# Kernel tuning notes

Measured on AMD Instinct MI355X. Metric: run time of the kernel, lower is better.

## Reference

```python
import jax, jax.numpy as jnp
from jax import lax
import numpy as np

B, H, W = 2, 48, 48
C_IN, C_OUT = 96, 192
D_INNER, N_STATE, DT_RANK, K = 192, 16, 6, 4  # VMamba: expand=2, d_state=16, dt_rank=ceil(C/16)
EPS = 1e-5


def setup_inputs() -> dict:
    ks = jax.random.split(jax.random.key(0), 16)
    s = 0.02
    r = lambda k, sh, sc=s: jax.random.normal(k, sh, jnp.float32) * sc
    d, N, R = D_INNER, N_STATE, DT_RANK
    return {
        "x": jax.random.normal(ks[0], (B, C_IN, H, W), jnp.float32),
        "ln_g": jnp.ones((C_IN,), jnp.float32),
        "ln_b": jnp.zeros((C_IN,), jnp.float32),
        "in_proj_w": r(ks[1], (2 * d, C_IN)),
        "dwconv_w": r(ks[2], (d, 1, 3, 3)),
        "dwconv_b": jnp.zeros((d,), jnp.float32),
        "x_proj_w": r(ks[3], (K, R + 2 * N, d)),
        "dt_w": r(ks[4], (K, d, R)),
        "dt_b": r(ks[5], (K, d), 0.1),
        "A_logs": jnp.tile(jnp.log(jnp.arange(1, N + 1, dtype=jnp.float32)), (K, d, 1)),
        "Ds": jnp.ones((K, d), jnp.float32),
        "out_norm_g": jnp.ones((d,), jnp.float32),
        "out_norm_b": jnp.zeros((d,), jnp.float32),
        "out_proj_w": r(ks[6], (C_IN, d)),
        "w1": r(ks[7], (C_OUT, C_IN, 1, 1)),
        "b1": jnp.zeros((C_OUT,), jnp.float32),
        "w31": r(ks[8], (C_OUT, C_IN, 3, 3)),
        "b31": jnp.zeros((C_OUT,), jnp.float32),
        "w32": r(ks[9], (C_OUT, C_IN, 3, 3)),
        "b32": jnp.zeros((C_OUT,), jnp.float32),
        "w33": r(ks[10], (C_OUT, C_OUT, 3, 3)),
        "b33": jnp.zeros((C_OUT,), jnp.float32),
        "bn_g": jnp.ones((3 * C_OUT,), jnp.float32),
        "bn_b": jnp.zeros((3 * C_OUT,), jnp.float32),
        "bn_m": r(ks[11], (3 * C_OUT,), 0.1),
        "bn_v": jax.random.uniform(ks[12], (3 * C_OUT,), jnp.float32) + 0.5,
        "prelu_a": jnp.float32(0.25),
    }


def _layernorm(x, g, b):
    m = jnp.mean(x, -1, keepdims=True)
    v = jnp.var(x, -1, keepdims=True)
    return (x - m) * lax.rsqrt(v + EPS) * g + b


def _conv(x, w, b, stride, pad, groups=1):
    y = lax.conv_general_dilated(x, w, (stride, stride), [(pad, pad), (pad, pad)],
                                 dimension_numbers=("NCHW", "OIHW", "NCHW"),
                                 feature_group_count=groups)
    return y + b[None, :, None, None]


def _ss2d(x, in_proj_w, dwconv_w, dwconv_b, x_proj_w, dt_w, dt_b, A_logs, Ds,
          out_norm_g, out_norm_b, out_proj_w):
    # x: (B, H, W, C)
    Bb, Hh, Ww, C = x.shape
    d, N, R = D_INNER, N_STATE, DT_RANK
    L = Hh * Ww
    xz = jnp.einsum("bhwc,ec->bhwe", x, in_proj_w)  # (B,H,W,2d)
    xin, z = jnp.split(xz, 2, axis=-1)
    xc = jnp.transpose(xin, (0, 3, 1, 2))           # (B,d,H,W)
    xc = jax.nn.silu(_conv(xc, dwconv_w, dwconv_b, 1, 1, groups=d))
    # 4 scan directions: row-major, col-major, and their reverses
    x_flat = xc.reshape(Bb, d, L)
    x_t = jnp.transpose(xc, (0, 1, 3, 2)).reshape(Bb, d, L)
    xs = jnp.stack([x_flat, x_t, x_flat[:, :, ::-1], x_t[:, :, ::-1]], axis=1)  # (B,K,d,L)
    x_dbl = jnp.einsum("bkdl,kcd->bkcl", xs, x_proj_w)
    dts, Bs, Cs = x_dbl[:, :, :R], x_dbl[:, :, R:R + N], x_dbl[:, :, R + N:]
    delta = jax.nn.softplus(jnp.einsum("bkrl,kdr->bkdl", dts, dt_w) + dt_b[None, :, :, None])
    A = -jnp.exp(A_logs)                                   # (K,d,N)
    dA = jnp.exp(jnp.einsum("bkdl,kdn->lbkdn", delta, A))  # (L,B,K,d,N)
    dBu = jnp.einsum("bkdl,bknl,bkdl->lbkdn", delta, Bs, xs)
    Cseq = jnp.transpose(Cs, (3, 0, 1, 2))                 # (L,B,K,N)

    def step(h, inp):
        dA_t, dBu_t, c_t = inp
        h = dA_t * h + dBu_t
        return h, jnp.einsum("bkdn,bkn->bkd", h, c_t)

    h0 = jnp.zeros((Bb, K, d, N), x.dtype)
    _, ys = lax.scan(step, h0, (dA, dBu, Cseq))            # ys: (L,B,K,d)
    ys = jnp.transpose(ys, (1, 2, 3, 0)) + xs * Ds[None, :, :, None]  # (B,K,d,L)

    def t_back(a):  # undo the HW transpose of col-major scans
        return jnp.transpose(a.reshape(Bb, d, Ww, Hh), (0, 1, 3, 2)).reshape(Bb, d, L)

    y = ys[:, 0] + ys[:, 2, :, ::-1] + t_back(ys[:, 1]) + t_back(ys[:, 3, :, ::-1])
    y = _layernorm(jnp.transpose(y, (0, 2, 1)), out_norm_g, out_norm_b).reshape(Bb, Hh, Ww, d)
    y = y * jax.nn.silu(z)
    return jnp.einsum("bhwd,cd->bhwc", y, out_proj_w)


def reference(x, ln_g, ln_b, in_proj_w, dwconv_w, dwconv_b, x_proj_w, dt_w, dt_b,
              A_logs, Ds, out_norm_g, out_norm_b, out_proj_w,
              w1, b1, w31, b31, w32, b32, w33, b33,
              bn_g, bn_b, bn_m, bn_v, prelu_a):
    # VSSBlock: residual + SS2D on LayerNorm'd NHWC features
    x_nhwc = jnp.transpose(x, (0, 2, 3, 1))
    x_nhwc = x_nhwc + _ss2d(_layernorm(x_nhwc, ln_g, ln_b), in_proj_w, dwconv_w,
                            dwconv_b, x_proj_w, dt_w, dt_b, A_logs, Ds,
                            out_norm_g, out_norm_b, out_proj_w)
    xm = jnp.transpose(x_nhwc, (0, 3, 1, 2))  # (B,C,H,W)
    # multi-branch stride-2 downsample
    x1 = _conv(xm, w1, b1, 2, 0)
    x2 = _conv(xm, w31, b31, 2, 1)
    x3 = _conv(_conv(xm, w32, b32, 2, 1), w33, b33, 1, 1)
    out = jnp.concatenate([x1, x2, x3], axis=1)  # (B, 3*C_OUT, H/2, W/2)
    # BatchNorm2d (inference, running stats) + PReLU(single param)
    out = (out - bn_m[None, :, None, None]) * lax.rsqrt(bn_v + EPS)[None, :, None, None] \
          * bn_g[None, :, None, None] + bn_b[None, :, None, None]
    return jnp.where(out > 0, out, prelu_a * out)
```

## Files before the change

### kernel.cpp

```cpp
#include <hip/hip_runtime.h>
#include <math.h>

#define BB_ 2
#define HH 48
#define WW 48
#define LL 2304
#define CIN 96
#define DD 192
#define KK 4
#define NN 16
#define RR 6
#define NCH 96
#define LC 24
#define COUT 192
#define OH 24
#define OW 24
#define OHW 576
#define NPX 1152
#define NTOT 4608
#define EPSF 1e-5f

typedef __attribute__((ext_vector_type(8))) short bf16x8;
typedef __attribute__((ext_vector_type(4))) float f32x4;

__device__ __forceinline__ short f2bf(float f) {
  unsigned u = __float_as_uint(f);
  unsigned r = (u + 0x7fffu + ((u >> 16) & 1u)) >> 16;
  return (short)r;
}

__global__ __launch_bounds__(256) void k_prep(const float* __restrict__ x,
                                              const float* __restrict__ g,
                                              const float* __restrict__ b,
                                              const float* __restrict__ inw,
                                              const float* __restrict__ xpw,
                                              const float* __restrict__ w31,
                                              const float* __restrict__ w32,
                                              const float* __restrict__ w33,
                                              const float* __restrict__ w1,
                                              const float* __restrict__ wout,
                                              float* __restrict__ stats,
                                              float* __restrict__ WgT,
                                              float* __restrict__ sWg,
                                              float* __restrict__ sWb,
                                              short* __restrict__ At3b,
                                              short* __restrict__ At1b,
                                              short* __restrict__ At2b,
                                              short* __restrict__ woutb) {
  int bx = blockIdx.x;
  int tid = threadIdx.x;
  if (bx < 72) {
    int bb = bx / 36; int l0 = (bx % 36) * 64;
    int p = tid >> 2, q = tid & 3;
    int l = l0 + p;
    const float* xp = x + bb * CIN * LL + l;
    float s = 0.f, ss = 0.f;
    for (int c = q; c < CIN; c += 4) { float v = xp[c * LL]; s += v; ss += v * v; }
    s += __shfl_xor(s, 1, 64); s += __shfl_xor(s, 2, 64);
    ss += __shfl_xor(ss, 1, 64); ss += __shfl_xor(ss, 2, 64);
    if (q == 0) {
      float m = s / CIN; float var = ss / CIN - m * m;
      stats[(bb * LL + l) * 2 + 0] = m;
      stats[(bb * LL + l) * 2 + 1] = rsqrtf(var + EPSF);
    }
  } else if (bx == 72) {
    for (int e = tid; e < 2 * DD; e += 256) {
      float swg = 0.f, swb = 0.f;
      for (int c = 0; c < CIN; c++) {
        float w = inw[e * CIN + c];
        float wg = w * g[c];
        WgT[c * 384 + e] = wg;
        swg += wg; swb += w * b[c];
      }
      sWg[e] = swg; sWb[e] = swb;
    }
  } else if (bx < 217) {
    int idx = (bx - 73) * 256 + tid;
    if (idx < 192 * 192) {
      int m = idx / 192;
      At3b[idx] = (m < 152) ? f2bf(xpw[idx]) : (short)0;
    }
  } else if (bx < 2161) {
    int i = (bx - 217) * 256 + tid;
    if (i < 497664) {
      float v;
      if (i < 165888) v = w31[i];
      else if (i < 331776) v = w32[i - 165888];
      else {
        int k = i % 864; int m = i / 864 - 384;
        v = (k % 9 == 4) ? w1[m * 96 + k / 9] : 0.f;
      }
      At1b[i] = f2bf(v);
    }
  } else if (bx < 3457) {
    int i = (bx - 2161) * 256 + tid;
    if (i < 331776) At2b[i] = f2bf(w33[i]);
  } else {
    int i = (bx - 3457) * 256 + tid;
    if (i < 18432) woutb[i] = f2bf(wout[i]);
  }
}

__global__ __launch_bounds__(256) void k_dwconv(const float* __restrict__ xin,
                                                const float* __restrict__ wdw,
                                                const float* __restrict__ bdw,
                                                float* __restrict__ xs,
                                                short* __restrict__ xsb) {
  __shared__ float vt[32 * 50];
  int bid = blockIdx.x;
  int bb = bid / 288; int r = bid % 288; int dg = r / 72; int tile = r % 72;
  int l0 = tile * 32;
  int d0 = dg * 48;
  for (int i = threadIdx.x; i < 32 * 48; i += 256) {
    int lj = i & 31, dl = i >> 5;
    int d = d0 + dl;
    int l = l0 + lj;
    int h = l / WW, w = l % WW;
    const float* xp = xin + (bb * DD + d) * LL;
    const float* wq = wdw + d * 9;
    float acc = bdw[d];
#pragma unroll
    for (int kh = 0; kh < 3; kh++) {
      int ih = h + kh - 1; if (ih < 0 || ih >= HH) continue;
#pragma unroll
      for (int kw = 0; kw < 3; kw++) {
        int iw = w + kw - 1; if (iw < 0 || iw >= WW) continue;
        acc += xp[ih * WW + iw] * wq[kh * 3 + kw];
      }
    }
    float v = acc / (1.f + __expf(-acc));
    vt[lj * 50 + dl] = v;
  }
  __syncthreads();
  for (int j = threadIdx.x; j < 32 * 48; j += 256) {
    int lj = j / 48, dl = j - lj * 48;
    int d = d0 + dl;
    int l = l0 + lj;
    int h = l / WW, w = l % WW;
    int lt = w * HH + h;
    float v = vt[lj * 50 + dl];
    xs[((size_t)(bb * 2 + 0) * LL + l) * DD + d] = v;
    xs[((size_t)(bb * 2 + 1) * LL + lt) * DD + d] = v;
    xsb[((size_t)bb * LL + l) * DD + d] = f2bf(v);
  }
}

__global__ __launch_bounds__(256) void k_xprojF(const short* __restrict__ At3b,
                                                const short* __restrict__ xsb,
                                                const float* __restrict__ dtw,
                                                const float* __restrict__ dtb,
                                                float* __restrict__ Bsb,
                                                float* __restrict__ Csb,
                                                float* __restrict__ delta) {
  __shared__ short As[192][40];
  __shared__ short Bs[32][40];
  __shared__ float ct[152][33];
  int p0 = blockIdx.x * 32;
  int tid = threadIdx.x;
  int lane = tid & 63;
  int wv = tid >> 6;
  int row16 = lane & 15;
  int kg = lane >> 4;
  f32x4 acc[3][2];
#pragma unroll
  for (int j = 0; j < 3; j++)
#pragma unroll
    for (int nf = 0; nf < 2; nf++) acc[j][nf] = (f32x4){0.f, 0.f, 0.f, 0.f};
  for (int ks = 0; ks < 192; ks += 32) {
#pragma unroll
    for (int it = 0; it < 3; it++) {
      int slot = tid + 256 * it;
      int sm = slot >> 2, sk8 = (slot & 3) * 8;
      *(bf16x8*)&As[sm][sk8] = *(const bf16x8*)&At3b[(size_t)sm * 192 + ks + sk8];
    }
    if (tid < 128) {
      int sn = tid >> 2, sk8 = (tid & 3) * 8;
      *(bf16x8*)&Bs[sn][sk8] = *(const bf16x8*)&xsb[(size_t)(p0 + sn) * 192 + ks + sk8];
    }
    __syncthreads();
#pragma unroll
    for (int j = 0; j < 3; j++) {
      bf16x8 a = *(const bf16x8*)&As[(wv * 3 + j) * 16 + row16][kg * 8];
#pragma unroll
      for (int nf = 0; nf < 2; nf++) {
        bf16x8 b = *(const bf16x8*)&Bs[nf * 16 + row16][kg * 8];
        acc[j][nf] = __builtin_amdgcn_mfma_f32_16x16x32_bf16(a, b, acc[j][nf], 0, 0, 0);
      }
    }
    __syncthreads();
  }
#pragma unroll
  for (int j = 0; j < 3; j++) {
    int rowb = (wv * 3 + j) * 16 + kg * 4;
#pragma unroll
    for (int nf = 0; nf < 2; nf++) {
      int col = nf * 16 + row16;
#pragma unroll
      for (int i = 0; i < 4; i++) {
        int r = rowb + i;
        if (r < 152) ct[r][col] = acc[j][nf][i];
      }
    }
  }
  __syncthreads();
  int bb = p0 / LL;
  int lbase = p0 - bb * LL;
  for (int i = tid; i < 2048; i += 256) {
    int k = i >> 9; int rem = i & 511; int lj = rem >> 4; int n = rem & 15;
    int l = lbase + lj; int h = l / WW, w = l - h * WW; int lt = w * HH + h;
    int pos = (k == 0) ? l : (k == 1) ? lt : (k == 2) ? (LL - 1 - l) : (LL - 1 - lt);
    size_t base = ((size_t)(bb * 4 + k) * LL + pos) * NN + n;
    Bsb[base] = ct[k * 38 + 6 + n][lj];
    Csb[base] = ct[k * 38 + 22 + n][lj];
  }
  for (int k = 0; k < 4; k++) {
    for (int i = tid; i < 32 * 192; i += 256) {
      int lj = i / 192, d = i - lj * 192;
      int l = lbase + lj; int h = l / WW, w = l - h * WW; int lt = w * HH + h;
      int pos = (k == 0) ? l : (k == 1) ? lt : (k == 2) ? (LL - 1 - l) : (LL - 1 - lt);
      const float* wd = dtw + (k * DD + d) * RR;
      float a2 = dtb[k * DD + d];
#pragma unroll
      for (int r = 0; r < RR; r++) a2 += wd[r] * ct[k * 38 + r][lj];
      float sp = a2 > 20.f ? a2 : log1pf(__expf(a2));
      delta[((size_t)(bb * 4 + k) * LL + pos) * DD + d] = sp;
    }
  }
}

__global__ __launch_bounds__(192) void k_scan1(const float* __restrict__ delta,
                                               const float* __restrict__ xs,
                                               const float* __restrict__ Bsb,
                                               const float* __restrict__ A_logs,
                                               float* __restrict__ Pbuf,
                                               float* __restrict__ Sbuf) {
  __shared__ float Bls[LC * NN];
  int bid = blockIdx.x;
  int c = bid % NCH; int bk = bid / NCH; int k = bk & 3; int bb = bk >> 2;
  int t0 = c * LC;
  int d = threadIdx.x;
  const float* bp = Bsb + ((size_t)bk * LL + t0) * NN;
  for (int i = d; i < LC * NN; i += 192) Bls[i] = bp[i];
  float A[NN];
  {
    const float4* ap = (const float4*)(A_logs + (k * DD + d) * NN);
#pragma unroll
    for (int j = 0; j < 4; j++) {
      float4 a4 = ap[j];
      A[4 * j + 0] = -__expf(a4.x); A[4 * j + 1] = -__expf(a4.y);
      A[4 * j + 2] = -__expf(a4.z); A[4 * j + 3] = -__expf(a4.w);
    }
  }
  bool seq = true;
#pragma unroll
  for (int n = 0; n < NN; n++) seq = seq && (fabsf(A[n] + (float)(n + 1)) < 1e-3f);
  float h[NN];
#pragma unroll
  for (int n = 0; n < NN; n++) h[n] = 0.f;
  float sd = 0.f;
  __syncthreads();
  const float* dp = delta + ((size_t)bk * LL + t0) * DD + d;
  const float* xpb = xs + ((size_t)(bb * 2 + (k & 1)) * LL) * DD + d;
  const float* xp; int xstep;
  if (k < 2) { xp = xpb + (size_t)t0 * DD; xstep = DD; }
  else       { xp = xpb + (size_t)(LL - 1 - t0) * DD; xstep = -DD; }
#pragma unroll 2
  for (int t = 0; t < LC; ++t) {
    float dt = dp[t * DD];
    float xv = xp[t * xstep];
    float u = dt * xv;
    sd += dt;
    float dA[NN];
    if (seq) {
      float q = __expf(-dt);
      float q2 = q * q, q4 = q2 * q2, q8 = q4 * q4;
      dA[0] = q; dA[1] = q2; dA[2] = q2 * q; dA[3] = q4;
      dA[4] = q4 * q; dA[5] = q4 * q2; dA[6] = q4 * dA[2]; dA[7] = q8;
      dA[8] = q8 * q; dA[9] = q8 * q2; dA[10] = q8 * dA[2]; dA[11] = q8 * q4;
      dA[12] = q8 * dA[4]; dA[13] = q8 * dA[5]; dA[14] = q8 * dA[6]; dA[15] = q8 * q8;
    } else {
#pragma unroll
      for (int n = 0; n < NN; n++) dA[n] = __expf(dt * A[n]);
    }
    const float4* b4 = (const float4*)&Bls[t * NN];
#pragma unroll
    for (int j = 0; j < 4; j++) {
      float4 bv = b4[j];
      h[4 * j + 0] = dA[4 * j + 0] * h[4 * j + 0] + u * bv.x;
      h[4 * j + 1] = dA[4 * j + 1] * h[4 * j + 1] + u * bv.y;
      h[4 * j + 2] = dA[4 * j + 2] * h[4 * j + 2] + u * bv.z;
      h[4 * j + 3] = dA[4 * j + 3] * h[4 * j + 3] + u * bv.w;
    }
  }
  int chn = (bk * DD + d) * NN;
  float* pp = Pbuf + (size_t)c * 24576 + chn;
  float* sp = Sbuf + (size_t)c * 24576 + chn;
#pragma unroll
  for (int n = 0; n < NN; n++) { pp[n] = __expf(A[n] * sd); sp[n] = h[n]; }
}

__global__ __launch_bounds__(256) void k_scan2(const float* __restrict__ Pbuf,
                                               const float* __restrict__ Sbuf,
                                               float* __restrict__ Hinit) {
  int idx = blockIdx.x * 256 + threadIdx.x;
  float h = 0.f;
  for (int c = 0; c < NCH; c++) {
    Hinit[(size_t)c * 24576 + idx] = h;
    h = Pbuf[(size_t)c * 24576 + idx] * h + Sbuf[(size_t)c * 24576 + idx];
  }
}

__global__ __launch_bounds__(192) void k_scan3(const float* __restrict__ delta,
                                               const float* __restrict__ xs,
                                               const float* __restrict__ Bsb,
                                               const float* __restrict__ Csb,
                                               const float* __restrict__ A_logs,
                                               const float* __restrict__ Ds,
                                               const float* __restrict__ Hinit,
                                               float* __restrict__ ys) {
  __shared__ float Bls[LC * NN];
  __shared__ float Cls[LC * NN];
  int bid = blockIdx.x;
  int c = bid % NCH; int bk = bid / NCH; int k = bk & 3; int bb = bk >> 2;
  int t0 = c * LC;
  int d = threadIdx.x;
  const float* bp = Bsb + ((size_t)bk * LL + t0) * NN;
  const float* cp = Csb + ((size_t)bk * LL + t0) * NN;
  for (int i = d; i < LC * NN; i += 192) { Bls[i] = bp[i]; Cls[i] = cp[i]; }
  float A[NN];
  {
    const float4* ap = (const float4*)(A_logs + (k * DD + d) * NN);
#pragma unroll
    for (int j = 0; j < 4; j++) {
      float4 a4 = ap[j];
      A[4 * j + 0] = -__expf(a4.x); A[4 * j + 1] = -__expf(a4.y);
      A[4 * j + 2] = -__expf(a4.z); A[4 * j + 3] = -__expf(a4.w);
    }
  }
  bool seq = true;
#pragma unroll
  for (int n = 0; n < NN; n++) seq = seq && (fabsf(A[n] + (float)(n + 1)) < 1e-3f);
  float Dv = Ds[k * DD + d];
  float h[NN];
  {
    const float4* hp = (const float4*)(Hinit + (size_t)c * 24576 + (bk * DD + d) * NN);
#pragma unroll
    for (int j = 0; j < 4; j++) {
      float4 h4 = hp[j];
      h[4 * j + 0] = h4.x; h[4 * j + 1] = h4.y;
      h[4 * j + 2] = h4.z; h[4 * j + 3] = h4.w;
    }
  }
  __syncthreads();
  const float* dp = delta + ((size_t)bk * LL + t0) * DD + d;
  const float* xpb = xs + ((size_t)(bb * 2 + (k & 1)) * LL) * DD + d;
  const float* xp; int xstep;
  if (k < 2) { xp = xpb + (size_t)t0 * DD; xstep = DD; }
  else       { xp = xpb + (size_t)(LL - 1 - t0) * DD; xstep = -DD; }
  float* yp = ys + ((size_t)bk * LL + t0) * DD + d;
#pragma unroll 2
  for (int t = 0; t < LC; ++t) {
    float dt = dp[t * DD];
    float xv = xp[t * xstep];
    float u = dt * xv;
    float y = 0.f;
    float dA[NN];
    if (seq) {
      float q = __expf(-dt);
      float q2 = q * q, q4 = q2 * q2, q8 = q4 * q4;
      dA[0] = q; dA[1] = q2; dA[2] = q2 * q; dA[3] = q4;
      dA[4] = q4 * q; dA[5] = q4 * q2; dA[6] = q4 * dA[2]; dA[7] = q8;
      dA[8] = q8 * q; dA[9] = q8 * q2; dA[10] = q8 * dA[2]; dA[11] = q8 * q4;
      dA[12] = q8 * dA[4]; dA[13] = q8 * dA[5]; dA[14] = q8 * dA[6]; dA[15] = q8 * q8;
    } else {
#pragma unroll
      for (int n = 0; n < NN; n++) dA[n] = __expf(dt * A[n]);
    }
    const float4* b4 = (const float4*)&Bls[t * NN];
    const float4* c4 = (const float4*)&Cls[t * NN];
#pragma unroll
    for (int j = 0; j < 4; j++) {
      float4 bv = b4[j];
      float4 cc = c4[j];
      h[4 * j + 0] = dA[4 * j + 0] * h[4 * j + 0] + u * bv.x;
      h[4 * j + 1] = dA[4 * j + 1] * h[4 * j + 1] + u * bv.y;
      h[4 * j + 2] = dA[4 * j + 2] * h[4 * j + 2] + u * bv.z;
      h[4 * j + 3] = dA[4 * j + 3] * h[4 * j + 3] + u * bv.w;
      y += h[4 * j + 0] * cc.x + h[4 * j + 1] * cc.y
         + h[4 * j + 2] * cc.z + h[4 * j + 3] * cc.w;
    }
    yp[t * DD] = y + Dv * xv;
  }
}

__global__ __launch_bounds__(256) void k_combineF(const float* __restrict__ ys,
                                                  const float* __restrict__ z,
                                                  const float* __restrict__ ong,
                                                  const float* __restrict__ onb,
                                                  const short* __restrict__ Wbf,
                                                  const float* __restrict__ x,
                                                  float* __restrict__ xm) {
  __shared__ float yt[32 * 194];
  __shared__ unsigned Wlu[96 * 98];
  int bx = blockIdx.x; int bb = bx / 72; int l0 = (bx % 72) * 32;
  int tid = threadIdx.x;
  const unsigned* Wu = (const unsigned*)Wbf;
  for (int i = tid; i < 96 * 96; i += 256) {
    int e = i / 96, d2 = i - e * 96;
    Wlu[e * 98 + d2] = Wu[i];
  }
  for (int i = tid; i < 32 * DD; i += 256) {
    int p = i / DD, d = i - p * DD;
    int l = l0 + p; int h = l / WW, w = l - h * WW;
    int t1 = w * HH + h;
    float v = ys[(((size_t)bb * KK + 0) * LL + l) * DD + d]
            + ys[(((size_t)bb * KK + 1) * LL + t1) * DD + d]
            + ys[(((size_t)bb * KK + 2) * LL + (LL - 1 - l)) * DD + d]
            + ys[(((size_t)bb * KK + 3) * LL + (LL - 1 - t1)) * DD + d];
    yt[p * 194 + d] = v;
  }
  __syncthreads();
  int p = tid >> 3, q = tid & 7;
  int l = l0 + p;
  float s = 0.f, ss = 0.f;
  for (int d = q * 24; d < q * 24 + 24; d++) { float v = yt[p * 194 + d]; s += v; ss += v * v; }
  s += __shfl_xor(s, 1, 64); s += __shfl_xor(s, 2, 64); s += __shfl_xor(s, 4, 64);
  ss += __shfl_xor(ss, 1, 64); ss += __shfl_xor(ss, 2, 64); ss += __shfl_xor(ss, 4, 64);
  float m = s / DD, var = ss / DD - m * m;
  float rr = rsqrtf(var + EPSF);
  const float* zp = z + (bb * LL + l) * DD;
  for (int d = q * 24; d < q * 24 + 24; d++) {
    float v = (yt[p * 194 + d] - m) * rr * ong[d] + onb[d];
    float zv = zp[d];
    yt[p * 194 + d] = v * zv / (1.f + __expf(-zv));
  }
  __syncthreads();
  float acc[12];
#pragma unroll
  for (int j = 0; j < 12; j++) acc[j] = 0.f;
  for (int d2 = 0; d2 < 96; d2++) {
    float2 y2 = *(float2*)&yt[p * 194 + 2 * d2];
#pragma unroll
    for (int j = 0; j < 12; j++) {
      unsigned wv = Wlu[(q * 12 + j) * 98 + d2];
      float wlo = __uint_as_float(wv << 16);
      float whi = __uint_as_float(wv & 0xffff0000u);
      acc[j] += y2.x * wlo + y2.y * whi;
    }
  }
#pragma unroll
  for (int j = 0; j < 12; j++) {
    int e = q * 12 + j;
    size_t off = ((size_t)bb * CIN + e) * LL + l;
    xm[off] = x[off] + acc[j];
  }
}

template<int MT, int KTOT, int KCHUNK, int CI, int IH, int STRIDE>
__global__ __launch_bounds__(256) void k_cgemm_mfma(const short* __restrict__ Abf,
                                                    const float* __restrict__ SRC,
                                                    float* __restrict__ Cout) {
  __shared__ short As[64][40];
  __shared__ short Bs[64][40];
  int n0 = blockIdx.x * 64;
  int m0 = blockIdx.y * 64;
  int kz = blockIdx.z;
  int k0 = kz * KCHUNK;
  int tid = threadIdx.x;
  int lane = tid & 63;
  int wv = tid >> 6;
  int row16 = lane & 15;
  int kg = lane >> 4;
  int sm = tid >> 2;
  int sk8 = (tid & 3) * 8;
  int n = n0 + sm;
  int bb = n / OHW; int rem = n - bb * OHW;
  int oh = rem / OW, ow = rem - oh * OW;
  f32x4 acc[4];
#pragma unroll
  for (int i = 0; i < 4; i++) acc[i] = (f32x4){0.f, 0.f, 0.f, 0.f};
  for (int ks = 0; ks < KCHUNK; ks += 32) {
    *(bf16x8*)&As[sm][sk8] =
        *(const bf16x8*)&Abf[(size_t)(m0 + sm) * KTOT + k0 + ks + sk8];
    bf16x8 bvv;
#pragma unroll
    for (int j = 0; j < 8; j++) {
      int k = k0 + ks + sk8 + j;
      int ci = k / 9; int r9 = k - ci * 9;
      int kh = r9 / 3, kw = r9 - kh * 3;
      int ih = STRIDE * oh + kh - 1;
      int iw = STRIDE * ow + kw - 1;
      float v = (ih >= 0 && ih < IH && iw >= 0 && iw < IH)
              ? SRC[((size_t)(bb * CI + ci) * IH + ih) * IH + iw] : 0.f;
      bvv[j] = f2bf(v);
    }
    *(bf16x8*)&Bs[sm][sk8] = bvv;
    __syncthreads();
    bf16x8 a = *(const bf16x8*)&As[wv * 16 + row16][kg * 8];
#pragma unroll
    for (int tn = 0; tn < 4; tn++) {
      bf16x8 b = *(const bf16x8*)&Bs[tn * 16 + row16][kg * 8];
      acc[tn] = __builtin_amdgcn_mfma_f32_16x16x32_bf16(a, b, acc[tn], 0, 0, 0);
    }
    __syncthreads();
  }
#pragma unroll
  for (int tn = 0; tn < 4; tn++) {
    int col = n0 + tn * 16 + row16;
    int rowb = m0 + wv * 16 + kg * 4;
#pragma unroll
    for (int i = 0; i < 4; i++)
      Cout[((size_t)kz * MT + rowb + i) * NPX + col] = acc[tn][i];
  }
}

template<int MT, int KD>
__global__ __launch_bounds__(256) void k_gemmF(const float* __restrict__ At,
                                               const float* __restrict__ Bm,
                                               int ldb, int boffB,
                                               float* __restrict__ C0,
                                               int ldc, int boffC,
                                               const float* __restrict__ a0,
                                               const float* __restrict__ a1,
                                               const float* __restrict__ a2,
                                               float* __restrict__ a3) {
  __shared__ float As[16][64];
  __shared__ float Bs[16][64];
  int n0 = blockIdx.x * 64;
  int m0 = blockIdx.y * 64;
  int bb = blockIdx.z;
  const float* B = Bm + (size_t)bb * boffB;
  int tid = threadIdx.x;
  int lr = tid >> 4;
  int lc = (tid & 15) * 4;
  int tm = tid >> 4;
  int tn = tid & 15;
  float acc[4][4] = {};
  for (int ks = 0; ks < KD; ks += 16) {
    *(float4*)&As[lr][lc] = *(const float4*)&At[(ks + lr) * MT + m0 + lc];
    *(float4*)&Bs[lr][lc] = *(const float4*)&B[(size_t)(ks + lr) * ldb + n0 + lc];
    __syncthreads();
#pragma unroll
    for (int kk = 0; kk < 16; kk++) {
      float4 a = *(float4*)&As[kk][tm * 4];
      float4 b = *(float4*)&Bs[kk][tn * 4];
      acc[0][0] += a.x * b.x; acc[0][1] += a.x * b.y; acc[0][2] += a.x * b.z; acc[0][3] += a.x * b.w;
      acc[1][0] += a.y * b.x; acc[1][1] += a.y * b.y; acc[1][2] += a.y * b.z; acc[1][3] += a.y * b.w;
      acc[2][0] += a.z * b.x; acc[2][1] += a.z * b.y; acc[2][2] += a.z * b.z; acc[2][3] += a.z * b.w;
      acc[3][0] += a.w * b.x; acc[3][1] += a.w * b.y; acc[3][2] += a.w * b.z; acc[3][3] += a.w * b.w;
    }
    __syncthreads();
  }
  int n = n0 + tn * 4;
  float m_[4], r_[4];
#pragma unroll
  for (int j = 0; j < 4; j++) {
    m_[j] = a0[((size_t)bb * LL + n + j) * 2];
    r_[j] = a0[((size_t)bb * LL + n + j) * 2 + 1];
  }
#pragma unroll
  for (int i = 0; i < 4; i++) {
    int e = m0 + tm * 4 + i;
    float swg = a1[e], swb = a2[e];
    float v0 = r_[0] * (acc[i][0] - m_[0] * swg) + swb;
    float v1 = r_[1] * (acc[i][1] - m_[1] * swg) + swb;
    float v2 = r_[2] * (acc[i][2] - m_[2] * swg) + swb;
    float v3 = r_[3] * (acc[i][3] - m_[3] * swg) + swb;
    if (e < DD) {
      float4 v = {v0, v1, v2, v3};
      *(float4*)&C0[(size_t)bb * boffC + (size_t)e * ldc + n] = v;
    } else {
      a3[((size_t)bb * LL + n + 0) * DD + (e - DD)] = v0;
      a3[((size_t)bb * LL + n + 1) * DD + (e - DD)] = v1;
      a3[((size_t)bb * LL + n + 2) * DD + (e - DD)] = v2;
      a3[((size_t)bb * LL + n + 3) * DD + (e - DD)] = v3;
    }
  }
}

__global__ __launch_bounds__(256) void k_reduce1(const float* __restrict__ Cp1,
                                                 const float* __restrict__ b1,
                                                 const float* __restrict__ b31,
                                                 const float* __restrict__ b32,
                                                 const float* __restrict__ bn_g,
                                                 const float* __restrict__ bn_b,
                                                 const float* __restrict__ bn_m,
                                                 const float* __restrict__ bn_v,
                                                 const float* __restrict__ prelu_a,
                                                 float* __restrict__ out,
                                                 float* __restrict__ t3) {
  int idx = blockIdx.x * 256 + threadIdx.x;
  if (idx >= 576 * NPX) return;
  int m = idx / NPX, n = idx % NPX;
  float s = 0.f;
#pragma unroll
  for (int c = 0; c < 3; c++) s += Cp1[(size_t)c * 576 * NPX + idx];
  int bb = n / OHW, o = n % OHW;
  if (m < 192) {
    s += b31[m];
    int cc = 192 + m;
    float scale = rsqrtf(bn_v[cc] + EPSF) * bn_g[cc];
    float v = s * scale + (bn_b[cc] - bn_m[cc] * scale);
    float a = prelu_a[0];
    out[((size_t)bb * 576 + cc) * OHW + o] = v > 0.f ? v : a * v;
  } else if (m < 384) {
    s += b32[m - 192];
    t3[((size_t)bb * COUT + (m - 192)) * OHW + o] = s;
  } else {
    s += b1[m - 384];
    int cc = m - 384;
    float scale = rsqrtf(bn_v[cc] + EPSF) * bn_g[cc];
    float v = s * scale + (bn_b[cc] - bn_m[cc] * scale);
    float a = prelu_a[0];
    out[((size_t)bb * 576 + cc) * OHW + o] = v > 0.f ? v : a * v;
  }
}

__global__ __launch_bounds__(256) void k_reduce2(const float* __restrict__ Cp2,
                                                 const float* __restrict__ b33,
                                                 const float* __restrict__ bn_g,
                                                 const float* __restrict__ bn_b,
                                                 const float* __restrict__ bn_m,
                                                 const float* __restrict__ bn_v,
                                                 const float* __restrict__ prelu_a,
                                                 float* __restrict__ out) {
  int idx = blockIdx.x * 256 + threadIdx.x;
  if (idx >= 192 * NPX) return;
  int m = idx / NPX, n = idx % NPX;
  float s = b33[m];
#pragma unroll
  for (int c = 0; c < 6; c++) s += Cp2[(size_t)c * 192 * NPX + idx];
  int bb = n / OHW, o = n % OHW;
  int cc = 384 + m;
  float scale = rsqrtf(bn_v[cc] + EPSF) * bn_g[cc];
  float v = s * scale + (bn_b[cc] - bn_m[cc] * scale);
  float a = prelu_a[0];
  out[((size_t)bb * 576 + cc) * OHW + o] = v > 0.f ? v : a * v;
}

extern "C" void kernel_launch(void* const* d_in, const int* in_sizes, int n_in,
                              void* d_out, int out_size, void* d_ws, size_t ws_size,
                              hipStream_t stream) {
  const float* x        = (const float*)d_in[0];
  const float* ln_g     = (const float*)d_in[1];
  const float* ln_b     = (const float*)d_in[2];
  const float* in_proj_w= (const float*)d_in[3];
  const float* dwconv_w = (const float*)d_in[4];
  const float* dwconv_b = (const float*)d_in[5];
  const float* x_proj_w = (const float*)d_in[6];
  const float* dt_w     = (const float*)d_in[7];
  const float* dt_b     = (const float*)d_in[8];
  const float* A_logs   = (const float*)d_in[9];
  const float* Ds       = (const float*)d_in[10];
  const float* out_norm_g = (const float*)d_in[11];
  const float* out_norm_b = (const float*)d_in[12];
  const float* out_proj_w = (const float*)d_in[13];
  const float* w1  = (const float*)d_in[14];
  const float* b1  = (const float*)d_in[15];
  const float* w31 = (const float*)d_in[16];
  const float* b31 = (const float*)d_in[17];
  const float* w32 = (const float*)d_in[18];
  const float* b32 = (const float*)d_in[19];
  const float* w33 = (const float*)d_in[20];
  const float* b33 = (const float*)d_in[21];
  const float* bn_g = (const float*)d_in[22];
  const float* bn_b = (const float*)d_in[23];
  const float* bn_m = (const float*)d_in[24];
  const float* bn_v = (const float*)d_in[25];
  const float* prelu_a = (const float*)d_in[26];

  float* ws = (float*)d_ws;
  float* stats = ws + 0;
  float* WgT   = ws + 16384;
  float* sWg   = ws + 65536;
  float* sWb   = ws + 66048;
  short* At3b  = (short*)(ws + 98304);
  short* At1b  = (short*)(ws + 147456);
  short* At2b  = (short*)(ws + 397312);
  short* woutb = (short*)(ws + 565248);
  float* xin   = ws + 2097152;
  float* z     = ws + 3145728;
  float* xs    = ws + 4194304;
  short* xsb   = (short*)(ws + 6291456);
  float* delta = ws + 10485760;
  float* Bsb   = ws + 14155776;
  float* Csb   = ws + 14680064;
  float* Pbuf  = ws + 15728640;
  float* Sbuf  = ws + 18874368;
  float* Hinit = ws + 22020096;
  float* ys    = ws + 25165824;
  float* xm    = ws + 29360128;
  float* t3    = ws + 30408704;
  float* Cp1   = ws + 31457280;
  float* Cp2   = ws + 33554432;
  float* out = (float*)d_out;

  k_prep<<<3529, 256, 0, stream>>>(x, ln_g, ln_b, in_proj_w, x_proj_w,
                                   w31, w32, w33, w1, out_proj_w,
                                   stats, WgT, sWg, sWb, At3b, At1b, At2b, woutb);
  k_gemmF<384, 96><<<dim3(36, 6, 2), 256, 0, stream>>>(
      WgT, x, LL, CIN * LL, xin, LL, DD * LL, stats, sWg, sWb, z);
  k_dwconv<<<576, 256, 0, stream>>>(xin, dwconv_w, dwconv_b, xs, xsb);
  k_xprojF<<<144, 256, 0, stream>>>(At3b, xsb, dt_w, dt_b, Bsb, Csb, delta);
  k_scan1<<<768, 192, 0, stream>>>(delta, xs, Bsb, A_logs, Pbuf, Sbuf);
  k_scan2<<<96, 256, 0, stream>>>(Pbuf, Sbuf, Hinit);
  k_scan3<<<768, 192, 0, stream>>>(delta, xs, Bsb, Csb, A_logs, Ds, Hinit, ys);
  k_combineF<<<144, 256, 0, stream>>>(ys, z, out_norm_g, out_norm_b, woutb, x, xm);
  k_cgemm_mfma<576, 864, 288, CIN, HH, 2><<<dim3(18, 9, 3), 256, 0, stream>>>(
      At1b, xm, Cp1);
  k_reduce1<<<2592, 256, 0, stream>>>(Cp1, b1, b31, b32, bn_g, bn_b, bn_m, bn_v,
                                      prelu_a, out, t3);
  k_cgemm_mfma<192, 1728, 288, COUT, OH, 1><<<dim3(18, 3, 6), 256, 0, stream>>>(
      At2b, t3, Cp2);
  k_reduce2<<<864, 256, 0, stream>>>(Cp2, b33, bn_g, bn_b, bn_m, bn_v, prelu_a, out);
}
```

Baseline: 206.1 us.

## Split x_proj kernel per scan direction with padded weight layout

The x_proj/dt kernel is repartitioned so that each block handles one scan direction for a 64-pixel tile. Previously each block covered all four directions for 32 pixels. The weights are repacked at prep time into four 48-row slabs (38 real rows padded), so each block's MFMA covers only its own direction's rows. This doubles the grid to 288 blocks and splits the heavy delta softplus/store loop across more blocks to improve occupancy. In exchange, each xsb tile is loaded four times (once per direction) and there is some padding overhead.

```diff
diff --git a/kernel.cpp b/kernel.cpp
--- a/kernel.cpp
+++ b/kernel.cpp
@@ -43,7 +43,7 @@
                                               float* __restrict__ WgT,
                                               float* __restrict__ sWg,
                                               float* __restrict__ sWb,
-                                              short* __restrict__ At3b,
+                                              short* __restrict__ At3p,
                                               short* __restrict__ At1b,
                                               short* __restrict__ At2b,
                                               short* __restrict__ woutb) {
@@ -76,9 +76,10 @@
     }
   } else if (bx < 217) {
     int idx = (bx - 73) * 256 + tid;
-    if (idx < 192 * 192) {
-      int m = idx / 192;
-      At3b[idx] = (m < 152) ? f2bf(xpw[idx]) : (short)0;
+    if (idx < 4 * 48 * 192) {
+      int m = idx / 192, d = idx - m * 192;
+      int kd = m / 48, r = m - kd * 48;
+      At3p[idx] = (r < 38) ? f2bf(xpw[(kd * 38 + r) * 192 + d]) : (short)0;
     }
   } else if (bx < 2161) {
     int i = (bx - 217) * 256 + tid;
@@ -145,86 +146,72 @@
   }
 }
 
-__global__ __launch_bounds__(256) void k_xprojF(const short* __restrict__ At3b,
+__global__ __launch_bounds__(256) void k_xprojF(const short* __restrict__ At3p,
                                                 const short* __restrict__ xsb,
                                                 const float* __restrict__ dtw,
                                                 const float* __restrict__ dtb,
                                                 float* __restrict__ Bsb,
                                                 float* __restrict__ Csb,
                                                 float* __restrict__ delta) {
-  __shared__ short As[192][40];
-  __shared__ short Bs[32][40];
-  __shared__ float ct[152][33];
-  int p0 = blockIdx.x * 32;
+  __shared__ short As[48][40];
+  __shared__ short Bs[64][40];
+  __shared__ float ct[38][65];
+  int bid = blockIdx.x;
+  int kd = bid / 72; int tile = bid % 72;
+  int pg0 = tile * 64;
+  int bb = pg0 / LL;
+  int lbase = pg0 - bb * LL;
   int tid = threadIdx.x;
   int lane = tid & 63;
-  int wv = tid >> 6;
+  int wvn = tid >> 6;
   int row16 = lane & 15;
   int kg = lane >> 4;
-  f32x4 acc[3][2];
-#pragma unroll
-  for (int j = 0; j < 3; j++)
-#pragma unroll
-    for (int nf = 0; nf < 2; nf++) acc[j][nf] = (f32x4){0.f, 0.f, 0.f, 0.f};
+  f32x4 acc[3];
+#pragma unroll
+  for (int j = 0; j < 3; j++) acc[j] = (f32x4){0.f, 0.f, 0.f, 0.f};
+  int sm = tid >> 2, sk8 = (tid & 3) * 8;
   for (int ks = 0; ks < 192; ks += 32) {
-#pragma unroll
-    for (int it = 0; it < 3; it++) {
-      int slot = tid + 256 * it;
-      int sm = slot >> 2, sk8 = (slot & 3) * 8;
-      *(bf16x8*)&As[sm][sk8] = *(const bf16x8*)&At3b[(size_t)sm * 192 + ks + sk8];
-    }
-    if (tid < 128) {
-      int sn = tid >> 2, sk8 = (tid & 3) * 8;
-      *(bf16x8*)&Bs[sn][sk8] = *(const bf16x8*)&xsb[(size_t)(p0 + sn) * 192 + ks + sk8];
-    }
+    if (tid < 192)
+      *(bf16x8*)&As[sm][sk8] =
+          *(const bf16x8*)&At3p[(size_t)(kd * 48 + sm) * 192 + ks + sk8];
+    *(bf16x8*)&Bs[sm][sk8] =
+        *(const bf16x8*)&xsb[(size_t)(pg0 + sm) * 192 + ks + sk8];
     __syncthreads();
+    bf16x8 b = *(const bf16x8*)&Bs[wvn * 16 + row16][kg * 8];
 #pragma unroll
     for (int j = 0; j < 3; j++) {
-      bf16x8 a = *(const bf16x8*)&As[(wv * 3 + j) * 16 + row16][kg * 8];
-#pragma unroll
-      for (int nf = 0; nf < 2; nf++) {
-        bf16x8 b = *(const bf16x8*)&Bs[nf * 16 + row16][kg * 8];
-        acc[j][nf] = __builtin_amdgcn_mfma_f32_16x16x32_bf16(a, b, acc[j][nf], 0, 0, 0);
-      }
+      bf16x8 a = *(const bf16x8*)&As[j * 16 + row16][kg * 8];
+      acc[j] = __builtin_amdgcn_mfma_f32_16x16x32_bf16(a, b, acc[j], 0, 0, 0);
     }
     __syncthreads();
   }
 #pragma unroll
   for (int j = 0; j < 3; j++) {
-    int rowb = (wv * 3 + j) * 16 + kg * 4;
-#pragma unroll
-    for (int nf = 0; nf < 2; nf++) {
-      int col = nf * 16 + row16;
-#pragma unroll
-      for (int i = 0; i < 4; i++) {
-        int r = rowb + i;
-        if (r < 152) ct[r][col] = acc[j][nf][i];
-      }
-    }
+    int rowb = j * 16 + kg * 4;
+    int col = wvn * 16 + row16;
+#pragma unroll
+    for (int i = 0; i < 4; i++)
+      if (rowb + i < 38) ct[rowb + i][col] = acc[j][i];
   }
   __syncthreads();
-  int bb = p0 / LL;
-  int lbase = p0 - bb * LL;
-  for (int i = tid; i < 2048; i += 256) {
-    int k = i >> 9; int rem = i & 511; int lj = rem >> 4; int n = rem & 15;
+  for (int i = tid; i < 64 * 16; i += 256) {
+    int lj = i >> 4, n = i & 15;
     int l = lbase + lj; int h = l / WW, w = l - h * WW; int lt = w * HH + h;
-    int pos = (k == 0) ? l : (k == 1) ? lt : (k == 2) ? (LL - 1 - l) : (LL - 1 - lt);
-    size_t base = ((size_t)(bb * 4 + k) * LL + pos) * NN + n;
-    Bsb[base] = ct[k * 38 + 6 + n][lj];
-    Csb[base] = ct[k * 38 + 22 + n][lj];
-  }
-  for (int k = 0; k < 4; k++) {
-    for (int i = tid; i < 32 * 192; i += 256) {
-      int lj = i / 192, d = i - lj * 192;
-      int l = lbase + lj; int h = l / WW, w = l - h * WW; int lt = w * HH + h;
-      int pos = (k == 0) ? l : (k == 1) ? lt : (k == 2) ? (LL - 1 - l) : (LL - 1 - lt);
-      const float* wd = dtw + (k * DD + d) * RR;
-      float a2 = dtb[k * DD + d];
-#pragma unroll
-      for (int r = 0; r < RR; r++) a2 += wd[r] * ct[k * 38 + r][lj];
-      float sp = a2 > 20.f ? a2 : log1pf(__expf(a2));
-      delta[((size_t)(bb * 4 + k) * LL + pos) * DD + d] = sp;
-    }
+    int pos = (kd == 0) ? l : (kd == 1) ? lt : (kd == 2) ? (LL - 1 - l) : (LL - 1 - lt);
+    size_t base = ((size_t)(bb * 4 + kd) * LL + pos) * NN + n;
+    Bsb[base] = ct[6 + n][lj];
+    Csb[base] = ct[22 + n][lj];
+  }
+  for (int i = tid; i < 64 * 192; i += 256) {
+    int lj = i / 192, d = i - lj * 192;
+    int l = lbase + lj; int h = l / WW, w = l - h * WW; int lt = w * HH + h;
+    int pos = (kd == 0) ? l : (kd == 1) ? lt : (kd == 2) ? (LL - 1 - l) : (LL - 1 - lt);
+    const float* wd = dtw + (kd * DD + d) * RR;
+    float a2 = dtb[kd * DD + d];
+#pragma unroll
+    for (int r = 0; r < RR; r++) a2 += wd[r] * ct[r][lj];
+    float sp = a2 > 20.f ? a2 : log1pf(__expf(a2));
+    delta[((size_t)(bb * 4 + kd) * LL + pos) * DD + d] = sp;
   }
 }
 
@@ -674,7 +661,7 @@
   float* WgT   = ws + 16384;
   float* sWg   = ws + 65536;
   float* sWb   = ws + 66048;
-  short* At3b  = (short*)(ws + 98304);
+  short* At3p  = (short*)(ws + 98304);
   short* At1b  = (short*)(ws + 147456);
   short* At2b  = (short*)(ws + 397312);
   short* woutb = (short*)(ws + 565248);
@@ -697,11 +684,11 @@
 
   k_prep<<<3529, 256, 0, stream>>>(x, ln_g, ln_b, in_proj_w, x_proj_w,
                                    w31, w32, w33, w1, out_proj_w,
-                                   stats, WgT, sWg, sWb, At3b, At1b, At2b, woutb);
+                                   stats, WgT, sWg, sWb, At3p, At1b, At2b, woutb);
   k_gemmF<384, 96><<<dim3(36, 6, 2), 256, 0, stream>>>(
       WgT, x, LL, CIN * LL, xin, LL, DD * LL, stats, sWg, sWb, z);
   k_dwconv<<<576, 256, 0, stream>>>(xin, dwconv_w, dwconv_b, xs, xsb);
-  k_xprojF<<<144, 256, 0, stream>>>(At3b, xsb, dt_w, dt_b, Bsb, Csb, delta);
+  k_xprojF<<<288, 256, 0, stream>>>(At3p, xsb, dt_w, dt_b, Bsb, Csb, delta);
   k_scan1<<<768, 192, 0, stream>>>(delta, xs, Bsb, A_logs, Pbuf, Sbuf);
   k_scan2<<<96, 256, 0, stream>>>(Pbuf, Sbuf, Hinit);
   k_scan3<<<768, 192, 0, stream>>>(delta, xs, Bsb, Csb, A_logs, Ds, Hinit, ys);
```

After: 190.7 us. -7.4%, faster.
